# Performance work log

Hardware: AMD Instinct MI355X
Metric: run time of the kernel (lower is better)

## Reference

```python
import jax, jax.numpy as jnp
import numpy as np

T, B, OBS, H, ACT = 256, 1024, 256, 256, 64
SLOPE = 0.1


def setup_inputs() -> dict:
    key = jax.random.key(0)
    ks = jax.random.split(key, 20)
    stdv = 1.0 / np.sqrt(H)
    u = lambda k, shape: jax.random.uniform(k, shape, jnp.float32, -stdv, stdv)
    return {
        "x": jax.random.normal(ks[0], (T, B, OBS), jnp.float32),
        "noise1": jax.random.uniform(ks[1], (T, B, 1), jnp.float32),
        "noise2": jax.random.uniform(ks[2], (T, B, 1), jnp.float32),
        # FCEncoder: two Linear+ReLU layers
        "We1": u(ks[3], (OBS, H)), "be1": u(ks[4], (H,)),
        "We2": u(ks[5], (H, H)), "be2": u(ks[6], (H,)),
        # cell_1 (bottom): U_11 [bottom,4H+1], U_21 [top,4H+1], W_01 [H,4H+1], bias
        "U11_1": u(ks[7], (H, 4 * H + 1)), "U21_1": u(ks[8], (H, 4 * H + 1)),
        "W01_1": u(ks[9], (H, 4 * H + 1)), "b1": u(ks[10], (4 * H + 1,)),
        # cell_2 (top, last layer): no U_21
        "U11_2": u(ks[11], (H, 4 * H + 1)), "W01_2": u(ks[12], (H, 4 * H + 1)),
        "b2": u(ks[13], (4 * H + 1,)),
        "Wh": u(ks[14], (H, H)), "bh": u(ks[15], (H,)),
        "Wp": u(ks[16], (H, ACT)), "bp": u(ks[17], (ACT,)),
    }


def _trigger_train(z_hat, noise):
    # forward: (noise < z_hat).float(); backward: 0.1 * identity (straight-through)
    hard = (noise < z_hat).astype(z_hat.dtype)
    return jax.lax.stop_gradient(hard) + 0.1 * (z_hat - jax.lax.stop_gradient(z_hat))


def _gates(f_s):
    f = jax.nn.sigmoid(f_s[:, 0:H])
    i = jax.nn.sigmoid(f_s[:, H:2 * H])
    o = jax.nn.sigmoid(f_s[:, 2 * H:3 * H])
    g = jnp.tanh(f_s[:, 3 * H:4 * H])
    z_hat = jnp.clip((SLOPE * f_s[:, 4 * H:4 * H + 1] + 1.0) / 2.0, 0.05, 0.95)
    return f, i, o, g, z_hat


def reference(x, noise1, noise2, We1, be1, We2, be2,
              U11_1, U21_1, W01_1, b1, U11_2, W01_2, b2, Wh, bh, Wp, bp):
    # encoder over all timesteps at once (parallel_wrapper equivalent)
    xe = jax.nn.relu(jnp.einsum('tbi,ih->tbh', x, We1) + be1)
    xe = jax.nn.relu(jnp.einsum('tbi,ih->tbh', xe, We2) + be2)

    def step(carry, inp):
        h1, c1, z1, h2, c2 = carry
        xt, n1, n2 = inp
        # ---- cell 1 (not last layer; z_bottom = 1) ----
        fs1 = h1 @ W01_1 + z1 * (h2 @ U21_1) + xt @ U11_1 + b1
        f, i, o, g, zhat1 = _gates(fs1)
        c1n = f * c1 + i * g              # z_bottom == 1 everywhere
        h1n = o * jnp.tanh(c1n)
        z1n = _trigger_train(zhat1, n1)
        # ---- cell 2 (last layer; z_bottom = z1n, s_topdown = 0) ----
        fs2 = h2 @ W01_2 + z1n * (h1n @ U11_2) + b2
        f2, i2, o2, g2, zhat2 = _gates(fs2)
        c2n = (1.0 - z1n) * c2 + z1n * (f2 * c2 + i2 * g2)
        h2n = o2 * jnp.tanh(c2n)
        _ = _trigger_train(zhat2, n2)
        return (h1n, c1n, z1n, h2n, c2n), h2n

    zeros = jnp.zeros((B, H), jnp.float32)
    init = (zeros, zeros, jnp.ones((B, 1), jnp.float32), zeros, zeros)
    _, emb = jax.lax.scan(step, init, (xe, noise1, noise2))  # emb: [T,B,H]

    hid = jax.nn.relu(jnp.einsum('tbh,hk->tbk', emb, Wh) + bh)
    pred = jnp.tanh(jnp.einsum('tbh,ha->tba', hid, Wp) + bp)
    return pred
```

## Files before the change

### kernel.cpp

```cpp
#include <hip/hip_runtime.h>
#include <math.h>

typedef __attribute__((ext_vector_type(8))) _Float16 half8;
typedef __attribute__((ext_vector_type(4))) float    f32x4;
typedef unsigned long long u64;

#define NSTEP 256
#define CH    32
#define NCHUNK (NSTEP/CH)
#define NB    1024
#define HID   256
#define BH    262144
#define LK    40
#define LK1   776
#define INV2K 4.8828125e-4f

#define W1H_OFF 0
#define W1L_OFF 49664
#define AB_OFF  99328
#define W2_OFF  140288
#define PAN_OFF 150528
#define SEQ_SMEM 150784
#define EX_OFF  AB_OFF

__device__ __forceinline__ float sigf(float x){ return 1.f/(1.f+expf(-x)); }
__device__ __forceinline__ void splitf(float v, _Float16& h, _Float16& l){
    h = (_Float16)v; l = (_Float16)((v - (float)h)*2048.f);
}
union H2U { _Float16 h[2]; unsigned u; };

__global__ __launch_bounds__(256)
void wsplit_k(const float* __restrict__ s0, const float* __restrict__ s1,
              const float* __restrict__ s2, int K, int N, int ldn,
              int kb1, int kb2, _Float16* __restrict__ oh, _Float16* __restrict__ ol)
{
    int idx = blockIdx.x*256 + threadIdx.x;
    if (idx >= N*K) return;
    int n = idx / K, k = idx - n*K;
    const float* s = (k < kb1) ? &s0[(size_t)k*ldn]
                   : (k < kb2) ? &s1[(size_t)(k-kb1)*ldn]
                               : &s2[(size_t)(k-kb2)*ldn];
    float v = s[n];
    _Float16 h, l; splitf(v, h, l);
    oh[idx] = h; ol[idx] = l;
}

__global__ void wz_k(const float* __restrict__ W01, const float* __restrict__ U21,
                     const float* __restrict__ U11, float* __restrict__ wz)
{
    int k = blockIdx.x*256 + threadIdx.x;
    if (k >= 768) return;
    wz[k] = (k < 256) ? W01[(size_t)k*1025 + 1024]
          : (k < 512) ? U21[(size_t)(k-256)*1025 + 1024]
                      : U11[(size_t)(k-512)*1025 + 1024];
}

__global__ __launch_bounds__(256)
void init_k(_Float16* h1H, _Float16* h1L, _Float16* h2H, _Float16* h2L,
            float* c1g, float* c2g, unsigned* zr)
{
    int i = blockIdx.x*256 + threadIdx.x;
    h1H[i] = (_Float16)0.f; h1L[i] = (_Float16)0.f;
    h2H[i] = (_Float16)0.f; h2L[i] = (_Float16)0.f;
    c1g[i] = 0.f; c2g[i] = 0.f;
    if (i < NB) zr[i] = 1u;
}

template<int AIN, int AOUT, int NCOL>
__global__ __launch_bounds__(256)
void gemm_t(const float* __restrict__ Af,
            const _Float16* __restrict__ Ah_, const _Float16* __restrict__ Al_,
            const _Float16* __restrict__ Bh_, const _Float16* __restrict__ Bl_,
            const float* __restrict__ bias,
            _Float16* __restrict__ Oh, _Float16* __restrict__ Ol,
            float* __restrict__ Of)
{
    constexpr int NT = 8;
    __shared__ __align__(16) char smem[40960];

    const int tid  = threadIdx.x;
    const size_t R0 = (size_t)blockIdx.x*64;
    const int C0   = blockIdx.y*64;
    const int rh   = (tid>>6)&1, ch = tid>>7;
    const int lane = tid&63, lr = lane&15, kq = (lane>>4)<<3;
    const int arow = tid>>2, seg = tid&3;
    const size_t abase = (R0+arow)*256 + seg*8;
    const size_t wbase = (size_t)(C0 + (tid>>2))*256 + seg*8;

    f32x4 am[2][2], ax[2][2];
#pragma unroll
    for (int r=0;r<2;++r)
#pragma unroll
        for (int c=0;c<2;++c){ am[r][c]=(f32x4)0.f; ax[r][c]=(f32x4)0.f; }

    half8 rah, ral, rwh, rwl;
    auto load_tile = [&](int k0, half8& ah, half8& al, half8& wh, half8& wl) {
        if (AIN == 0) {
            float4 a0 = *(const float4*)(Af + abase + k0);
            float4 a1 = *(const float4*)(Af + abase + k0 + 4);
            float av[8] = {a0.x,a0.y,a0.z,a0.w,a1.x,a1.y,a1.z,a1.w};
#pragma unroll
            for (int i=0;i<8;++i){ _Float16 h,l; splitf(av[i],h,l); ah[i]=h; al[i]=l; }
        } else {
            ah = *(const half8*)(Ah_ + abase + k0);
            al = *(const half8*)(Al_ + abase + k0);
        }
        wh = *(const half8*)(Bh_ + wbase + k0);
        wl = *(const half8*)(Bl_ + wbase + k0);
    };
    auto store_tile = [&](int buf) {
        char* bs = smem + buf*20480;
        *(half8*)((_Float16*)(bs        ) + arow*LK + seg*8) = rah;
        *(half8*)((_Float16*)(bs +  5120) + arow*LK + seg*8) = ral;
        *(half8*)((_Float16*)(bs + 10240) + (tid>>2)*LK + seg*8) = rwh;
        *(half8*)((_Float16*)(bs + 15360) + (tid>>2)*LK + seg*8) = rwl;
    };

    load_tile(0, rah, ral, rwh, rwl);
    store_tile(0);

#pragma unroll 2
    for (int kb = 0; kb < NT; ++kb) {
        const int buf = kb & 1;
        half8 nah, nal, nwh, nwl;
        if (kb+1 < NT) load_tile((kb+1)*32, nah, nal, nwh, nwl);
        __syncthreads();
        const char* bs = smem + buf*20480;
        const _Float16* LAh = (const _Float16*)bs;
        const _Float16* LAl = (const _Float16*)(bs +  5120);
        const _Float16* LBh = (const _Float16*)(bs + 10240);
        const _Float16* LBl = (const _Float16*)(bs + 15360);
        half8 fah[2], fal[2], fbh[2], fbl[2];
#pragma unroll
        for (int rf=0;rf<2;++rf) {
            fah[rf] = *(const half8*)(LAh + (rh*32+rf*16+lr)*LK + kq);
            fal[rf] = *(const half8*)(LAl + (rh*32+rf*16+lr)*LK + kq);
        }
#pragma unroll
        for (int cf=0;cf<2;++cf) {
            fbh[cf] = *(const half8*)(LBh + (ch*32+cf*16+lr)*LK + kq);
            fbl[cf] = *(const half8*)(LBl + (ch*32+cf*16+lr)*LK + kq);
        }
#pragma unroll
        for (int cf=0;cf<2;++cf)
#pragma unroll
            for (int rf=0;rf<2;++rf) {
                am[rf][cf] = __builtin_amdgcn_mfma_f32_16x16x32_f16(fah[rf], fbh[cf], am[rf][cf],0,0,0);
                ax[rf][cf] = __builtin_amdgcn_mfma_f32_16x16x32_f16(fah[rf], fbl[cf], ax[rf][cf],0,0,0);
                ax[rf][cf] = __builtin_amdgcn_mfma_f32_16x16x32_f16(fal[rf], fbh[cf], ax[rf][cf],0,0,0);
            }
        if (kb+1 < NT) {
            rah=nah; ral=nal; rwh=nwh; rwl=nwl;
            store_tile((kb+1)&1);
        }
    }

#pragma unroll
    for (int cf=0;cf<2;++cf) {
        int col = C0 + ch*32 + cf*16 + lr;
        float bcol = bias[col];
#pragma unroll
        for (int rf=0;rf<2;++rf)
#pragma unroll
            for (int q=0;q<4;++q) {
                size_t row = R0 + rh*32 + rf*16 + ((lane>>4)<<2) + q;
                float v = am[rf][cf][q] + ax[rf][cf][q]*INV2K + bcol;
                if (AOUT == 0) {
                    v = fmaxf(v, 0.f);
                    _Float16 h,l; splitf(v,h,l);
                    Oh[row*NCOL + col] = h;
                    Ol[row*NCOL + col] = l;
                } else {
                    Of[row*NCOL + col] = tanhf(v);
                }
            }
    }
}

struct PArgs {
    const _Float16 *XeH, *XeL;
    _Float16 *EmH, *EmL;
    const _Float16 *W1h, *W1l, *W2h, *W2l;
    const float *b1, *b2, *wz, *noise;
    _Float16 *h1rH, *h1rL, *h2rH, *h2rL;
    unsigned *zr;
    float *c1g, *c2g;
    unsigned *ctr;
    unsigned *tick;
    int chunk;
};

__device__ __forceinline__ void xbarrier(unsigned* c, int tid)
{
    __syncthreads();
    if (tid == 0) {
        __hip_atomic_fetch_add(c, 1u, __ATOMIC_RELAXED, __HIP_MEMORY_SCOPE_AGENT);
        int guard = 0;
        while (__hip_atomic_load(c, __ATOMIC_RELAXED, __HIP_MEMORY_SCOPE_AGENT) < 32u
               && guard < (1<<16)) {
            __builtin_amdgcn_s_sleep(2);
            ++guard;
        }
    }
    __syncthreads();
}

__global__ __launch_bounds__(512, 1)
void hm_pers_k(PArgs a)
{
    extern __shared__ __align__(16) char smem[];

    const int tid = threadIdx.x, wv = tid>>6, lane = tid&63;

    unsigned* pan_sh = (unsigned*)(smem + PAN_OFF);
    if (tid == 0) {
        unsigned xcc;
        asm volatile("s_getreg_b32 %0, hwreg(HW_REG_XCC_ID)" : "=s"(xcc));
        xcc &= 7u;
        unsigned slot = __hip_atomic_fetch_add(a.tick + a.chunk*8 + xcc, 1u,
                          __ATOMIC_RELAXED, __HIP_MEMORY_SCOPE_AGENT);
        pan_sh[0] = xcc;
        pan_sh[1] = slot & 31u;
    }
    __syncthreads();
    const int panel = pan_sh[0], cs = pan_sh[1];

    const int rg = wv & 3, cg = wv >> 2;
    const int lr = lane & 15, kq = (lane>>4) << 3;
    const int R0 = panel * 128;
    const int j0h = cs * 8;
    const int srow = tid >> 2, seg = tid & 3;
    const size_t arbase = (size_t)(R0 + srow) * HID;
    const bool do_z = (cs == 0);

    const int fcl  = cg*16 + lr;
    const int gate = fcl >> 3;
    const int jc   = fcl & 7;
    const float bv1 = a.b1[gate*256 + j0h + jc];
    const float bv2 = a.b2[gate*256 + j0h + jc];

    const int hl2 = (tid >= 128) & 1;
    const int tt2 = tid & 127;
    const int fc2 = tt2 >> 2, sg2 = tt2 & 3;
    const _Float16* W2src = hl2 ? a.W2l : a.W2h;
    const size_t w2base = (size_t)((fc2>>3)*256 + j0h + (fc2&7))*512 + sg2*8;

#pragma unroll
    for (int it = 0; it < 12; ++it) {
        int idx = it*512 + tid;
        int hl  = idx >= 3072;
        int e   = idx - hl*3072;
        int fc  = e / 96;
        int ks  = e - fc*96;
        const _Float16* src = (hl ? a.W1l : a.W1h)
            + (size_t)((fc>>3)*256 + j0h + (fc&7))*768 + ks*8;
        *(half8*)(smem + (hl ? W1L_OFF : W1H_OFF) + (fc*LK1 + ks*8)*2)
            = *(const half8*)src;
    }
    __syncthreads();

    const int urow = tid >> 2, ujj = (tid & 3)*2;
    const size_t ubase = (size_t)(R0 + urow)*HID + j0h + ujj;

    float c1s[2], c2s[2];
    {
        float2 cv1 = *(const float2*)(a.c1g + ubase);
        float2 cv2 = *(const float2*)(a.c2g + ubase);
        c1s[0]=cv1.x; c1s[1]=cv1.y; c2s[0]=cv2.x; c2s[1]=cv2.y;
    }

    float* ex = (float*)(smem + EX_OFF);

#pragma unroll 1
    for (int s = 0; s < CH; ++s) {
        const int t = a.chunk*CH + s;
        const _Float16* h1cH = a.h1rH + (size_t)s*BH;
        const _Float16* h1cL = a.h1rL + (size_t)s*BH;
        _Float16*       h1nH = a.h1rH + (size_t)(s+1)*BH;
        _Float16*       h1nL = a.h1rL + (size_t)(s+1)*BH;
        const _Float16* h2cH = a.h2rH + (size_t)s*BH;
        const _Float16* h2cL = a.h2rL + (size_t)s*BH;
        _Float16*       h2nH = a.h2rH + (size_t)(s+1)*BH;
        _Float16*       h2nL = a.h2rL + (size_t)(s+1)*BH;
        const unsigned* zc = a.zr + (size_t)s*NB;
        unsigned*       zn = a.zr + (size_t)(s+1)*NB;
        const _Float16* xeh = a.XeH + (size_t)t*BH;
        const _Float16* xel = a.XeL + (size_t)t*BH;

        const unsigned zrv = zc[R0+srow];
        f32x4 am[2], ax[2];
        am[0]=(f32x4)0.f; am[1]=(f32x4)0.f; ax[0]=(f32x4)0.f; ax[1]=(f32x4)0.f;
        float zacc = 0.f;
        half8 rAh[2], rAl[2], rW[2];

        auto p1_load = [&](int kt, int sl){
            int kg = kt*32 + seg*8;
            half8 hv, lv;
            if (kg < 256)      { hv = *(const half8*)(h1cH + arbase + kg);
                                 lv = *(const half8*)(h1cL + arbase + kg); }
            else if (kg < 512) {
                if (zrv) { hv = *(const half8*)(h2cH + arbase + (kg-256));
                           lv = *(const half8*)(h2cL + arbase + (kg-256)); }
                else     { hv = half8{}; lv = half8{}; }
            } else             { hv = *(const half8*)(xeh + arbase + (kg-512));
                                 lv = *(const half8*)(xel + arbase + (kg-512)); }
            rAh[sl]=hv; rAl[sl]=lv;
        };
        auto stgA = [&](int buf, int sl){
            *(half8*)(smem + AB_OFF + buf*20480         + (srow*LK + seg*8)*2) = rAh[sl];
            *(half8*)(smem + AB_OFF + buf*20480 + 10240 + (srow*LK + seg*8)*2) = rAl[sl];
        };
        auto cmp1 = [&](int buf, int kt){
            const _Float16* LAh = (const _Float16*)(smem + AB_OFF + buf*20480);
            const _Float16* LAl = (const _Float16*)(smem + AB_OFF + buf*20480 + 10240);
            const int bo = fcl*LK1 + kt*32 + kq;
            half8 fbh = *(const half8*)((const _Float16*)(smem + W1H_OFF) + bo);
            half8 fbl = *(const half8*)((const _Float16*)(smem + W1L_OFF) + bo);
#pragma unroll
            for (int rf=0; rf<2; ++rf) {
                const int ao = (rg*32 + rf*16 + lr)*LK + kq;
                half8 fah = *(const half8*)(LAh + ao);
                half8 fal = *(const half8*)(LAl + ao);
                am[rf] = __builtin_amdgcn_mfma_f32_16x16x32_f16(fah, fbh, am[rf],0,0,0);
                ax[rf] = __builtin_amdgcn_mfma_f32_16x16x32_f16(fah, fbl, ax[rf],0,0,0);
                ax[rf] = __builtin_amdgcn_mfma_f32_16x16x32_f16(fal, fbh, ax[rf],0,0,0);
            }
            if (do_z) {
#pragma unroll
                for (int i=0;i<8;++i) {
                    float av = (float)LAh[srow*LK + seg*8 + i]
                             + (float)LAl[srow*LK + seg*8 + i]*INV2K;
                    zacc = fmaf(av, a.wz[kt*32 + seg*8 + i], zacc);
                }
            }
        };

        p1_load(0,0); p1_load(1,1);
        stgA(0,0);
#pragma unroll
        for (int kt = 0; kt < 24; ++kt) {
            if (kt+2 < 24) p1_load(kt+2, kt&1);
            __syncthreads();
            cmp1(kt&1, kt);
            if (kt+1 < 24) stgA((kt+1)&1, (kt+1)&1);
        }
        __syncthreads();

#pragma unroll
        for (int rf=0; rf<2; ++rf)
#pragma unroll
            for (int q=0;q<4;++q) {
                float v = am[rf][q] + ax[rf][q]*INV2K + bv1;
                v = (gate<3) ? sigf(v) : tanhf(v);
                int row = rg*32 + rf*16 + ((lane>>4)<<2) + q;
                ex[(gate*128 + row)*9 + jc] = v;
            }
        if (do_z) {
            float sum = zacc;
            sum += __shfl_xor(sum, 1);
            sum += __shfl_xor(sum, 2);
            if (seg == 0) {
                float fsz = sum + a.b1[1024];
                float zh = fminf(fmaxf((0.1f*fsz + 1.f)*0.5f, 0.05f), 0.95f);
                unsigned zv = (a.noise[(size_t)t*NB + R0+srow] < zh) ? 1u : 0u;
                zn[R0+srow] = zv;
                if (s == CH-1) a.zr[R0+srow] = zv;
            }
        }
        __syncthreads();
        {
            H2U hh, hl;
#pragma unroll
            for (int q=0;q<2;++q) {
                float f0 = ex[(0*128+urow)*9 + ujj + q];
                float i0 = ex[(1*128+urow)*9 + ujj + q];
                float o0 = ex[(2*128+urow)*9 + ujj + q];
                float g0 = ex[(3*128+urow)*9 + ujj + q];
                float cn = f0*c1s[q] + i0*g0;
                c1s[q] = cn;
                float hv = o0*tanhf(cn);
                _Float16 h,l; splitf(hv,h,l); hh.h[q]=h; hl.h[q]=l;
            }
            *(unsigned*)(h1nH + ubase) = hh.u;
            *(unsigned*)(h1nL + ubase) = hl.u;
            if (s == CH-1) {
                *(unsigned*)(a.h1rH + ubase) = hh.u;
                *(unsigned*)(a.h1rL + ubase) = hl.u;
            }
        }
        xbarrier(a.ctr + ((size_t)(a.chunk*CH + s)*2 + 0)*8 + panel, tid);

        const unsigned zrv2 = zn[R0+srow];
        am[0]=(f32x4)0.f; am[1]=(f32x4)0.f; ax[0]=(f32x4)0.f; ax[1]=(f32x4)0.f;

        auto p2_load = [&](int kt, int sl){
            int kg = kt*32 + seg*8;
            half8 hv, lv;
            if (kg < 256)      { hv = *(const half8*)(h2cH + arbase + kg);
                                 lv = *(const half8*)(h2cL + arbase + kg); }
            else {
                if (zrv2) { hv = *(const half8*)(h1nH + arbase + (kg-256));
                            lv = *(const half8*)(h1nL + arbase + (kg-256)); }
                else      { hv = half8{}; lv = half8{}; }
            }
            rAh[sl]=hv; rAl[sl]=lv;
            if (tid < 256) rW[sl] = *(const half8*)(W2src + w2base + kt*32);
        };
        auto stg2 = [&](int buf, int sl){
            *(half8*)(smem + AB_OFF + buf*20480         + (srow*LK + seg*8)*2) = rAh[sl];
            *(half8*)(smem + AB_OFF + buf*20480 + 10240 + (srow*LK + seg*8)*2) = rAl[sl];
            if (tid < 256)
                *(half8*)(smem + W2_OFF + buf*5120 + hl2*2560 + (fc2*LK + sg2*8)*2) = rW[sl];
        };
        auto cmp2 = [&](int buf){
            const _Float16* LAh = (const _Float16*)(smem + AB_OFF + buf*20480);
            const _Float16* LAl = (const _Float16*)(smem + AB_OFF + buf*20480 + 10240);
            const int bo = fcl*LK + kq;
            half8 fbh = *(const half8*)((const _Float16*)(smem + W2_OFF + buf*5120) + bo);
            half8 fbl = *(const half8*)((const _Float16*)(smem + W2_OFF + buf*5120 + 2560) + bo);
#pragma unroll
            for (int rf=0; rf<2; ++rf) {
                const int ao = (rg*32 + rf*16 + lr)*LK + kq;
                half8 fah = *(const half8*)(LAh + ao);
                half8 fal = *(const half8*)(LAl + ao);
                am[rf] = __builtin_amdgcn_mfma_f32_16x16x32_f16(fah, fbh, am[rf],0,0,0);
                ax[rf] = __builtin_amdgcn_mfma_f32_16x16x32_f16(fah, fbl, ax[rf],0,0,0);
                ax[rf] = __builtin_amdgcn_mfma_f32_16x16x32_f16(fal, fbh, ax[rf],0,0,0);
            }
        };

        p2_load(0,0); p2_load(1,1);
        stg2(0,0);
#pragma unroll
        for (int kt = 0; kt < 16; ++kt) {
            if (kt+2 < 16) p2_load(kt+2, kt&1);
            __syncthreads();
            cmp2(kt&1);
            if (kt+1 < 16) stg2((kt+1)&1, (kt+1)&1);
        }
        __syncthreads();

#pragma unroll
        for (int rf=0; rf<2; ++rf)
#pragma unroll
            for (int q=0;q<4;++q) {
                float v = am[rf][q] + ax[rf][q]*INV2K + bv2;
                v = (gate<3) ? sigf(v) : tanhf(v);
                int row = rg*32 + rf*16 + ((lane>>4)<<2) + q;
                ex[(gate*128 + row)*9 + jc] = v;
            }
        __syncthreads();
        {
            unsigned zun = zn[R0+urow];
            H2U hh, hl;
#pragma unroll
            for (int q=0;q<2;++q) {
                float f0 = ex[(0*128+urow)*9 + ujj + q];
                float i0 = ex[(1*128+urow)*9 + ujj + q];
                float o0 = ex[(2*128+urow)*9 + ujj + q];
                float g0 = ex[(3*128+urow)*9 + ujj + q];
                float cn = zun ? (f0*c2s[q] + i0*g0) : c2s[q];
                c2s[q] = cn;
                float hv = o0*tanhf(cn);
                _Float16 h,l; splitf(hv,h,l); hh.h[q]=h; hl.h[q]=l;
            }
            *(unsigned*)(h2nH + ubase) = hh.u;
            *(unsigned*)(h2nL + ubase) = hl.u;
            *(unsigned*)(a.EmH + (size_t)t*BH + ubase) = hh.u;
            *(unsigned*)(a.EmL + (size_t)t*BH + ubase) = hl.u;
            if (s == CH-1) {
                *(unsigned*)(a.h2rH + ubase) = hh.u;
                *(unsigned*)(a.h2rL + ubase) = hl.u;
            }
        }
        xbarrier(a.ctr + ((size_t)(a.chunk*CH + s)*2 + 1)*8 + panel, tid);
    }

    *(float2*)(a.c1g + ubase) = float2{c1s[0], c1s[1]};
    *(float2*)(a.c2g + ubase) = float2{c2s[0], c2s[1]};
}

extern "C" void kernel_launch(void* const* d_in, const int* in_sizes, int n_in,
                              void* d_out, int out_size, void* d_ws, size_t ws_size,
                              hipStream_t stream)
{
    const float* x     = (const float*)d_in[0];
    const float* n1    = (const float*)d_in[1];
    const float* We1   = (const float*)d_in[3];
    const float* be1   = (const float*)d_in[4];
    const float* We2   = (const float*)d_in[5];
    const float* be2   = (const float*)d_in[6];
    const float* U11_1 = (const float*)d_in[7];
    const float* U21_1 = (const float*)d_in[8];
    const float* W01_1 = (const float*)d_in[9];
    const float* b1    = (const float*)d_in[10];
    const float* U11_2 = (const float*)d_in[11];
    const float* W01_2 = (const float*)d_in[12];
    const float* b2    = (const float*)d_in[13];
    const float* Wh    = (const float*)d_in[14];
    const float* bh    = (const float*)d_in[15];
    const float* Wp    = (const float*)d_in[16];
    const float* bp_   = (const float*)d_in[17];
    float* out = (float*)d_out;

    char* p = (char*)d_ws;
    auto alloc = [&](size_t bytes){ char* q = p; p += (bytes + 255) & ~(size_t)255; return q; };
    _Float16* XeH  = (_Float16*)alloc((size_t)NSTEP*BH*2);
    _Float16* XeL  = (_Float16*)alloc((size_t)NSTEP*BH*2);
    _Float16* EmH  = (_Float16*)alloc((size_t)NSTEP*BH*2);
    _Float16* EmL  = (_Float16*)alloc((size_t)NSTEP*BH*2);
    _Float16* Wt1h = (_Float16*)alloc((size_t)1024*768*2);
    _Float16* Wt1l = (_Float16*)alloc((size_t)1024*768*2);
    _Float16* Wt2h = (_Float16*)alloc((size_t)1024*512*2);
    _Float16* Wt2l = (_Float16*)alloc((size_t)1024*512*2);
    _Float16* We1h = (_Float16*)alloc(256*256*2);
    _Float16* We1l = (_Float16*)alloc(256*256*2);
    _Float16* We2h = (_Float16*)alloc(256*256*2);
    _Float16* We2l = (_Float16*)alloc(256*256*2);
    _Float16* Whh  = (_Float16*)alloc(256*256*2);
    _Float16* Whl  = (_Float16*)alloc(256*256*2);
    _Float16* Wph  = (_Float16*)alloc(64*256*2);
    _Float16* Wpl  = (_Float16*)alloc(64*256*2);
    float*    wz1  = (float*)alloc(768*4);
    _Float16* h1rH = (_Float16*)alloc((size_t)(CH+1)*BH*2);
    _Float16* h1rL = (_Float16*)alloc((size_t)(CH+1)*BH*2);
    _Float16* h2rH = (_Float16*)alloc((size_t)(CH+1)*BH*2);
    _Float16* h2rL = (_Float16*)alloc((size_t)(CH+1)*BH*2);
    unsigned* zr   = (unsigned*)alloc((size_t)(CH+1)*NB*4);
    float*    c1g  = (float*)alloc((size_t)BH*4);
    float*    c2g  = (float*)alloc((size_t)BH*4);
    unsigned* ctr  = (unsigned*)alloc((size_t)NCHUNK*CH*2*8*4);
    unsigned* tick = (unsigned*)alloc((size_t)NCHUNK*8*4);
    if (ws_size < (size_t)(p - (char*)d_ws)) return;

    _Float16* TmpH = EmH; _Float16* TmpL = EmL;
    _Float16* TpH  = XeH; _Float16* TpL  = XeL;

    wsplit_k<<<dim3(3072), 256, 0, stream>>>(W01_1, U21_1, U11_1, 768, 1024, 1025, 256, 512, Wt1h, Wt1l);
    wsplit_k<<<dim3(2048), 256, 0, stream>>>(W01_2, U11_2, nullptr, 512, 1024, 1025, 256, 512, Wt2h, Wt2l);
    wsplit_k<<<dim3(256),  256, 0, stream>>>(We1, nullptr, nullptr, 256, 256, 256, 256, 256, We1h, We1l);
    wsplit_k<<<dim3(256),  256, 0, stream>>>(We2, nullptr, nullptr, 256, 256, 256, 256, 256, We2h, We2l);
    wsplit_k<<<dim3(256),  256, 0, stream>>>(Wh,  nullptr, nullptr, 256, 256, 256, 256, 256, Whh,  Whl);
    wsplit_k<<<dim3(64),   256, 0, stream>>>(Wp,  nullptr, nullptr, 256, 64, 64, 256, 256, Wph, Wpl);
    wz_k<<<dim3(3), 256, 0, stream>>>(W01_1, U21_1, U11_1, wz1);
    init_k<<<dim3(1024), 256, 0, stream>>>(h1rH, h1rL, h2rH, h2rL, c1g, c2g, zr);
    (void)hipMemsetAsync(ctr, 0, (size_t)NCHUNK*CH*2*8*4, stream);
    (void)hipMemsetAsync(tick, 0, (size_t)NCHUNK*8*4, stream);

    for (int c = 0; c < 8; ++c) {
        size_t ro = (size_t)c*32*BH;
        gemm_t<0,0,256><<<dim3(512,4), 256, 0, stream>>>(
            x + ro, nullptr, nullptr, We1h, We1l, be1, TmpH, TmpL, nullptr);
        gemm_t<1,0,256><<<dim3(512,4), 256, 0, stream>>>(
            nullptr, TmpH, TmpL, We2h, We2l, be2, XeH + ro, XeL + ro, nullptr);
    }

    (void)hipFuncSetAttribute((const void*)hm_pers_k,
        hipFuncAttributeMaxDynamicSharedMemorySize, SEQ_SMEM);
    PArgs pa;
    pa.XeH = XeH; pa.XeL = XeL; pa.EmH = EmH; pa.EmL = EmL;
    pa.W1h = Wt1h; pa.W1l = Wt1l; pa.W2h = Wt2h; pa.W2l = Wt2l;
    pa.b1 = b1; pa.b2 = b2; pa.wz = wz1; pa.noise = n1;
    pa.h1rH = h1rH; pa.h1rL = h1rL; pa.h2rH = h2rH; pa.h2rL = h2rL;
    pa.zr = zr; pa.c1g = c1g; pa.c2g = c2g; pa.ctr = ctr; pa.tick = tick;
    for (int c = 0; c < NCHUNK; ++c) {
        pa.chunk = c;
        void* kargs[] = { (void*)&pa };
        (void)hipLaunchCooperativeKernel((const void*)hm_pers_k, dim3(256), dim3(512),
                                         kargs, SEQ_SMEM, stream);
    }

    for (int c = 0; c < 8; ++c) {
        size_t ro = (size_t)c*32*BH;
        gemm_t<1,0,256><<<dim3(512,4), 256, 0, stream>>>(
            nullptr, EmH + ro, EmL + ro, Whh, Whl, bh, TpH, TpL, nullptr);
        gemm_t<1,1,64><<<dim3(512,1), 256, 0, stream>>>(
            nullptr, TpH, TpL, Wph, Wpl, bp_, nullptr, nullptr,
            out + (size_t)c*32*NB*64);
    }
}
```

Measured before the change: 7.312 ms.

## Interleave gate columns so each lane computes full LSTM cell in registers

Weight columns are permuted at split time so the four gates of one hidden unit land in adjacent MFMA output rows. Each wave now owns 16 batch rows and streams activations directly from global memory into MFMA operands, with no LDS staging of A tiles. The gate nonlinearity and cell update happen in registers without the LDS exchange buffer and the extra block barriers. Layer-2 high weights are kept in LDS while the low parts are read from global, and the z reduction runs as a separate pass. In exchange there are more redundant global loads and scalar 2-byte stores instead of packed stores.

Result: slower. 10.39 ms (+42.0%).

```diff
diff --git a/kernel.cpp b/kernel.cpp
--- a/kernel.cpp
+++ b/kernel.cpp
@@ -13,34 +13,34 @@
 #define BH    262144
 #define LK    40
 #define LK1   776
+#define LW2   520
 #define INV2K 4.8828125e-4f
 
 #define W1H_OFF 0
 #define W1L_OFF 49664
-#define AB_OFF  99328
-#define W2_OFF  140288
-#define PAN_OFF 150528
-#define SEQ_SMEM 150784
-#define EX_OFF  AB_OFF
+#define W2H_OFF 99328
+#define PAN_OFF 132608
+#define SEQ_SMEM 132864
 
 __device__ __forceinline__ float sigf(float x){ return 1.f/(1.f+expf(-x)); }
 __device__ __forceinline__ void splitf(float v, _Float16& h, _Float16& l){
     h = (_Float16)v; l = (_Float16)((v - (float)h)*2048.f);
 }
-union H2U { _Float16 h[2]; unsigned u; };
 
 __global__ __launch_bounds__(256)
 void wsplit_k(const float* __restrict__ s0, const float* __restrict__ s1,
               const float* __restrict__ s2, int K, int N, int ldn,
-              int kb1, int kb2, _Float16* __restrict__ oh, _Float16* __restrict__ ol)
+              int kb1, int kb2, int perm,
+              _Float16* __restrict__ oh, _Float16* __restrict__ ol)
 {
     int idx = blockIdx.x*256 + threadIdx.x;
     if (idx >= N*K) return;
     int n = idx / K, k = idx - n*K;
+    int jsrc = perm ? ((n&3)*256 + (n>>2)) : n;
     const float* s = (k < kb1) ? &s0[(size_t)k*ldn]
                    : (k < kb2) ? &s1[(size_t)(k-kb1)*ldn]
                                : &s2[(size_t)(k-kb2)*ldn];
-    float v = s[n];
+    float v = s[jsrc];
     _Float16 h, l; splitf(v, h, l);
     oh[idx] = h; ol[idx] = l;
 }
@@ -211,6 +211,7 @@
     extern __shared__ __align__(16) char smem[];
 
     const int tid = threadIdx.x, wv = tid>>6, lane = tid&63;
+    const int lr = lane&15, hq = lane>>4, kg8 = hq<<3;
 
     unsigned* pan_sh = (unsigned*)(smem + PAN_OFF);
     if (tid == 0) {
@@ -224,52 +225,51 @@
     }
     __syncthreads();
     const int panel = pan_sh[0], cs = pan_sh[1];
-
-    const int rg = wv & 3, cg = wv >> 2;
-    const int lr = lane & 15, kq = (lane>>4) << 3;
-    const int R0 = panel * 128;
-    const int j0h = cs * 8;
-    const int srow = tid >> 2, seg = tid & 3;
-    const size_t arbase = (size_t)(R0 + srow) * HID;
+    const int R0 = panel*128, hb = cs*8;
+    const int row = R0 + wv*16 + lr;
+    const size_t rbase = (size_t)row*HID;
     const bool do_z = (cs == 0);
-
-    const int fcl  = cg*16 + lr;
-    const int gate = fcl >> 3;
-    const int jc   = fcl & 7;
-    const float bv1 = a.b1[gate*256 + j0h + jc];
-    const float bv2 = a.b2[gate*256 + j0h + jc];
-
-    const int hl2 = (tid >= 128) & 1;
-    const int tt2 = tid & 127;
-    const int fc2 = tt2 >> 2, sg2 = tt2 & 3;
-    const _Float16* W2src = hl2 ? a.W2l : a.W2h;
-    const size_t w2base = (size_t)((fc2>>3)*256 + j0h + (fc2&7))*512 + sg2*8;
+    const int hc0 = hb + hq, hc1 = hb + 4 + hq;
+
+    float b1v[2][4], b2v[2][4];
+#pragma unroll
+    for (int cf=0; cf<2; ++cf)
+#pragma unroll
+        for (int q=0;q<4;++q) {
+            int hc = hb + cf*4 + hq;
+            b1v[cf][q] = a.b1[q*256 + hc];
+            b2v[cf][q] = a.b2[q*256 + hc];
+        }
 
 #pragma unroll
     for (int it = 0; it < 12; ++it) {
         int idx = it*512 + tid;
         int hl  = idx >= 3072;
         int e   = idx - hl*3072;
-        int fc  = e / 96;
-        int ks  = e - fc*96;
+        int c   = e / 96;
+        int ks  = e - c*96;
         const _Float16* src = (hl ? a.W1l : a.W1h)
-            + (size_t)((fc>>3)*256 + j0h + (fc&7))*768 + ks*8;
-        *(half8*)(smem + (hl ? W1L_OFF : W1H_OFF) + (fc*LK1 + ks*8)*2)
+            + (size_t)(cs*32 + c)*768 + ks*8;
+        *(half8*)(smem + (hl ? W1L_OFF : W1H_OFF) + (c*LK1 + ks*8)*2)
             = *(const half8*)src;
     }
+#pragma unroll
+    for (int it = 0; it < 4; ++it) {
+        int idx = it*512 + tid;
+        int c   = idx >> 6;
+        int ks  = idx & 63;
+        const _Float16* src = a.W2h + (size_t)(cs*32 + c)*512 + ks*8;
+        *(half8*)(smem + W2H_OFF + (c*LW2 + ks*8)*2) = *(const half8*)src;
+    }
     __syncthreads();
 
-    const int urow = tid >> 2, ujj = (tid & 3)*2;
-    const size_t ubase = (size_t)(R0 + urow)*HID + j0h + ujj;
-
-    float c1s[2], c2s[2];
-    {
-        float2 cv1 = *(const float2*)(a.c1g + ubase);
-        float2 cv2 = *(const float2*)(a.c2g + ubase);
-        c1s[0]=cv1.x; c1s[1]=cv1.y; c2s[0]=cv2.x; c2s[1]=cv2.y;
-    }
-
-    float* ex = (float*)(smem + EX_OFF);
+    float c1s[2] = { a.c1g[rbase + hc0], a.c1g[rbase + hc1] };
+    float c2s[2] = { a.c2g[rbase + hc0], a.c2g[rbase + hc1] };
+
+    const _Float16* w2lp[2] = {
+        a.W2l + (size_t)(cs*32      + lr)*512 + kg8,
+        a.W2l + (size_t)(cs*32 + 16 + lr)*512 + kg8
+    };
 
 #pragma unroll 1
     for (int s = 0; s < CH; ++s) {
@@ -287,197 +287,127 @@
         const _Float16* xeh = a.XeH + (size_t)t*BH;
         const _Float16* xel = a.XeL + (size_t)t*BH;
 
-        const unsigned zrv = zc[R0+srow];
+        const bool zrv = zc[row] != 0u;
         f32x4 am[2], ax[2];
         am[0]=(f32x4)0.f; am[1]=(f32x4)0.f; ax[0]=(f32x4)0.f; ax[1]=(f32x4)0.f;
-        float zacc = 0.f;
-        half8 rAh[2], rAl[2], rW[2];
-
-        auto p1_load = [&](int kt, int sl){
-            int kg = kt*32 + seg*8;
-            half8 hv, lv;
-            if (kg < 256)      { hv = *(const half8*)(h1cH + arbase + kg);
-                                 lv = *(const half8*)(h1cL + arbase + kg); }
-            else if (kg < 512) {
-                if (zrv) { hv = *(const half8*)(h2cH + arbase + (kg-256));
-                           lv = *(const half8*)(h2cL + arbase + (kg-256)); }
-                else     { hv = half8{}; lv = half8{}; }
-            } else             { hv = *(const half8*)(xeh + arbase + (kg-512));
-                                 lv = *(const half8*)(xel + arbase + (kg-512)); }
-            rAh[sl]=hv; rAl[sl]=lv;
-        };
-        auto stgA = [&](int buf, int sl){
-            *(half8*)(smem + AB_OFF + buf*20480         + (srow*LK + seg*8)*2) = rAh[sl];
-            *(half8*)(smem + AB_OFF + buf*20480 + 10240 + (srow*LK + seg*8)*2) = rAl[sl];
-        };
-        auto cmp1 = [&](int buf, int kt){
-            const _Float16* LAh = (const _Float16*)(smem + AB_OFF + buf*20480);
-            const _Float16* LAl = (const _Float16*)(smem + AB_OFF + buf*20480 + 10240);
-            const int bo = fcl*LK1 + kt*32 + kq;
-            half8 fbh = *(const half8*)((const _Float16*)(smem + W1H_OFF) + bo);
-            half8 fbl = *(const half8*)((const _Float16*)(smem + W1L_OFF) + bo);
-#pragma unroll
-            for (int rf=0; rf<2; ++rf) {
-                const int ao = (rg*32 + rf*16 + lr)*LK + kq;
-                half8 fah = *(const half8*)(LAh + ao);
-                half8 fal = *(const half8*)(LAl + ao);
-                am[rf] = __builtin_amdgcn_mfma_f32_16x16x32_f16(fah, fbh, am[rf],0,0,0);
-                ax[rf] = __builtin_amdgcn_mfma_f32_16x16x32_f16(fah, fbl, ax[rf],0,0,0);
-                ax[rf] = __builtin_amdgcn_mfma_f32_16x16x32_f16(fal, fbh, ax[rf],0,0,0);
+
+#pragma unroll
+        for (int kt = 0; kt < 24; ++kt) {
+            const int k0 = kt*32;
+            half8 sh, sl;
+            if (k0 < 256)      { sh = *(const half8*)(h1cH + rbase + k0 + kg8);
+                                 sl = *(const half8*)(h1cL + rbase + k0 + kg8); }
+            else if (k0 < 512) { sh = *(const half8*)(h2cH + rbase + (k0-256) + kg8);
+                                 sl = *(const half8*)(h2cL + rbase + (k0-256) + kg8);
+                                 if (!zrv) { sh = half8{}; sl = half8{}; } }
+            else               { sh = *(const half8*)(xeh + rbase + (k0-512) + kg8);
+                                 sl = *(const half8*)(xel + rbase + (k0-512) + kg8); }
+#pragma unroll
+            for (int cf = 0; cf < 2; ++cf) {
+                const int wb = (cf*16 + lr)*LK1 + k0 + kg8;
+                half8 wh = *(const half8*)((const _Float16*)(smem + W1H_OFF) + wb);
+                half8 wl = *(const half8*)((const _Float16*)(smem + W1L_OFF) + wb);
+                am[cf] = __builtin_amdgcn_mfma_f32_16x16x32_f16(wh, sh, am[cf],0,0,0);
+                ax[cf] = __builtin_amdgcn_mfma_f32_16x16x32_f16(wl, sh, ax[cf],0,0,0);
+                ax[cf] = __builtin_amdgcn_mfma_f32_16x16x32_f16(wh, sl, ax[cf],0,0,0);
             }
-            if (do_z) {
-#pragma unroll
-                for (int i=0;i<8;++i) {
-                    float av = (float)LAh[srow*LK + seg*8 + i]
-                             + (float)LAl[srow*LK + seg*8 + i]*INV2K;
-                    zacc = fmaf(av, a.wz[kt*32 + seg*8 + i], zacc);
-                }
+        }
+
+        if (do_z) {
+            const int srow = tid>>2, seg = tid&3;
+            const int grow = R0 + srow;
+            const size_t rb = (size_t)grow*HID;
+            const bool zrow_v = zc[grow] != 0u;
+            float zacc = 0.f;
+#pragma unroll
+            for (int kt = 0; kt < 24; ++kt) {
+                const int k0 = kt*32 + seg*8;
+                half8 hv, lv;
+                if (k0 < 256)      { hv = *(const half8*)(h1cH + rb + k0);
+                                     lv = *(const half8*)(h1cL + rb + k0); }
+                else if (k0 < 512) { hv = *(const half8*)(h2cH + rb + (k0-256));
+                                     lv = *(const half8*)(h2cL + rb + (k0-256));
+                                     if (!zrow_v) { hv = half8{}; lv = half8{}; } }
+                else               { hv = *(const half8*)(xeh + rb + (k0-512));
+                                     lv = *(const half8*)(xel + rb + (k0-512)); }
+#pragma unroll
+                for (int i=0;i<8;++i)
+                    zacc = fmaf((float)hv[i] + (float)lv[i]*INV2K,
+                                a.wz[k0 + i], zacc);
             }
-        };
-
-        p1_load(0,0); p1_load(1,1);
-        stgA(0,0);
-#pragma unroll
-        for (int kt = 0; kt < 24; ++kt) {
-            if (kt+2 < 24) p1_load(kt+2, kt&1);
-            __syncthreads();
-            cmp1(kt&1, kt);
-            if (kt+1 < 24) stgA((kt+1)&1, (kt+1)&1);
-        }
-        __syncthreads();
-
-#pragma unroll
-        for (int rf=0; rf<2; ++rf)
-#pragma unroll
-            for (int q=0;q<4;++q) {
-                float v = am[rf][q] + ax[rf][q]*INV2K + bv1;
-                v = (gate<3) ? sigf(v) : tanhf(v);
-                int row = rg*32 + rf*16 + ((lane>>4)<<2) + q;
-                ex[(gate*128 + row)*9 + jc] = v;
+            zacc += __shfl_xor(zacc, 1);
+            zacc += __shfl_xor(zacc, 2);
+            if (seg == 0) {
+                float fsz = zacc + a.b1[1024];
+                float zh = fminf(fmaxf((0.1f*fsz + 1.f)*0.5f, 0.05f), 0.95f);
+                unsigned zv = (a.noise[(size_t)t*NB + grow] < zh) ? 1u : 0u;
+                zn[grow] = zv;
+                if (s == CH-1) a.zr[grow] = zv;
             }
-        if (do_z) {
-            float sum = zacc;
-            sum += __shfl_xor(sum, 1);
-            sum += __shfl_xor(sum, 2);
-            if (seg == 0) {
-                float fsz = sum + a.b1[1024];
-                float zh = fminf(fmaxf((0.1f*fsz + 1.f)*0.5f, 0.05f), 0.95f);
-                unsigned zv = (a.noise[(size_t)t*NB + R0+srow] < zh) ? 1u : 0u;
-                zn[R0+srow] = zv;
-                if (s == CH-1) a.zr[R0+srow] = zv;
+        }
+
+#pragma unroll
+        for (int cf = 0; cf < 2; ++cf) {
+            float v0 = am[cf][0] + ax[cf][0]*INV2K + b1v[cf][0];
+            float v1 = am[cf][1] + ax[cf][1]*INV2K + b1v[cf][1];
+            float v2 = am[cf][2] + ax[cf][2]*INV2K + b1v[cf][2];
+            float v3 = am[cf][3] + ax[cf][3]*INV2K + b1v[cf][3];
+            float f = sigf(v0), i = sigf(v1), o = sigf(v2), g = tanhf(v3);
+            float cn = f*c1s[cf] + i*g;
+            c1s[cf] = cn;
+            float hn = o*tanhf(cn);
+            _Float16 hh, hl; splitf(hn, hh, hl);
+            const int hc = (cf==0) ? hc0 : hc1;
+            h1nH[rbase + hc] = hh; h1nL[rbase + hc] = hl;
+            if (s == CH-1) { a.h1rH[rbase + hc] = hh; a.h1rL[rbase + hc] = hl; }
+        }
+        xbarrier(a.ctr + ((size_t)(a.chunk*CH + s)*2 + 0)*8 + panel, tid);
+
+        const bool znv = zn[row] != 0u;
+        am[0]=(f32x4)0.f; am[1]=(f32x4)0.f; ax[0]=(f32x4)0.f; ax[1]=(f32x4)0.f;
+
+#pragma unroll
+        for (int kt = 0; kt < 16; ++kt) {
+            const int k0 = kt*32;
+            half8 sh, sl;
+            if (k0 < 256) { sh = *(const half8*)(h2cH + rbase + k0 + kg8);
+                            sl = *(const half8*)(h2cL + rbase + k0 + kg8); }
+            else          { sh = *(const half8*)(h1nH + rbase + (k0-256) + kg8);
+                            sl = *(const half8*)(h1nL + rbase + (k0-256) + kg8);
+                            if (!znv) { sh = half8{}; sl = half8{}; } }
+#pragma unroll
+            for (int cf = 0; cf < 2; ++cf) {
+                const int wb = (cf*16 + lr)*LW2 + k0 + kg8;
+                half8 wh = *(const half8*)((const _Float16*)(smem + W2H_OFF) + wb);
+                half8 wl = *(const half8*)(w2lp[cf] + k0);
+                am[cf] = __builtin_amdgcn_mfma_f32_16x16x32_f16(wh, sh, am[cf],0,0,0);
+                ax[cf] = __builtin_amdgcn_mfma_f32_16x16x32_f16(wl, sh, ax[cf],0,0,0);
+                ax[cf] = __builtin_amdgcn_mfma_f32_16x16x32_f16(wh, sl, ax[cf],0,0,0);
             }
         }
-        __syncthreads();
-        {
-            H2U hh, hl;
-#pragma unroll
-            for (int q=0;q<2;++q) {
-                float f0 = ex[(0*128+urow)*9 + ujj + q];
-                float i0 = ex[(1*128+urow)*9 + ujj + q];
-                float o0 = ex[(2*128+urow)*9 + ujj + q];
-                float g0 = ex[(3*128+urow)*9 + ujj + q];
-                float cn = f0*c1s[q] + i0*g0;
-                c1s[q] = cn;
-                float hv = o0*tanhf(cn);
-                _Float16 h,l; splitf(hv,h,l); hh.h[q]=h; hl.h[q]=l;
-            }
-            *(unsigned*)(h1nH + ubase) = hh.u;
-            *(unsigned*)(h1nL + ubase) = hl.u;
-            if (s == CH-1) {
-                *(unsigned*)(a.h1rH + ubase) = hh.u;
-                *(unsigned*)(a.h1rL + ubase) = hl.u;
-            }
-        }
-        xbarrier(a.ctr + ((size_t)(a.chunk*CH + s)*2 + 0)*8 + panel, tid);
-
-        const unsigned zrv2 = zn[R0+srow];
-        am[0]=(f32x4)0.f; am[1]=(f32x4)0.f; ax[0]=(f32x4)0.f; ax[1]=(f32x4)0.f;
-
-        auto p2_load = [&](int kt, int sl){
-            int kg = kt*32 + seg*8;
-            half8 hv, lv;
-            if (kg < 256)      { hv = *(const half8*)(h2cH + arbase + kg);
-                                 lv = *(const half8*)(h2cL + arbase + kg); }
-            else {
-                if (zrv2) { hv = *(const half8*)(h1nH + arbase + (kg-256));
-                            lv = *(const half8*)(h1nL + arbase + (kg-256)); }
-                else      { hv = half8{}; lv = half8{}; }
-            }
-            rAh[sl]=hv; rAl[sl]=lv;
-            if (tid < 256) rW[sl] = *(const half8*)(W2src + w2base + kt*32);
-        };
-        auto stg2 = [&](int buf, int sl){
-            *(half8*)(smem + AB_OFF + buf*20480         + (srow*LK + seg*8)*2) = rAh[sl];
-            *(half8*)(smem + AB_OFF + buf*20480 + 10240 + (srow*LK + seg*8)*2) = rAl[sl];
-            if (tid < 256)
-                *(half8*)(smem + W2_OFF + buf*5120 + hl2*2560 + (fc2*LK + sg2*8)*2) = rW[sl];
-        };
-        auto cmp2 = [&](int buf){
-            const _Float16* LAh = (const _Float16*)(smem + AB_OFF + buf*20480);
-            const _Float16* LAl = (const _Float16*)(smem + AB_OFF + buf*20480 + 10240);
-            const int bo = fcl*LK + kq;
-            half8 fbh = *(const half8*)((const _Float16*)(smem + W2_OFF + buf*5120) + bo);
-            half8 fbl = *(const half8*)((const _Float16*)(smem + W2_OFF + buf*5120 + 2560) + bo);
-#pragma unroll
-            for (int rf=0; rf<2; ++rf) {
-                const int ao = (rg*32 + rf*16 + lr)*LK + kq;
-                half8 fah = *(const half8*)(LAh + ao);
-                half8 fal = *(const half8*)(LAl + ao);
-                am[rf] = __builtin_amdgcn_mfma_f32_16x16x32_f16(fah, fbh, am[rf],0,0,0);
-                ax[rf] = __builtin_amdgcn_mfma_f32_16x16x32_f16(fah, fbl, ax[rf],0,0,0);
-                ax[rf] = __builtin_amdgcn_mfma_f32_16x16x32_f16(fal, fbh, ax[rf],0,0,0);
-            }
-        };
-
-        p2_load(0,0); p2_load(1,1);
-        stg2(0,0);
-#pragma unroll
-        for (int kt = 0; kt < 16; ++kt) {
-            if (kt+2 < 16) p2_load(kt+2, kt&1);
-            __syncthreads();
-            cmp2(kt&1);
-            if (kt+1 < 16) stg2((kt+1)&1, (kt+1)&1);
-        }
-        __syncthreads();
-
-#pragma unroll
-        for (int rf=0; rf<2; ++rf)
-#pragma unroll
-            for (int q=0;q<4;++q) {
-                float v = am[rf][q] + ax[rf][q]*INV2K + bv2;
-                v = (gate<3) ? sigf(v) : tanhf(v);
-                int row = rg*32 + rf*16 + ((lane>>4)<<2) + q;
-                ex[(gate*128 + row)*9 + jc] = v;
-            }
-        __syncthreads();
-        {
-            unsigned zun = zn[R0+urow];
-            H2U hh, hl;
-#pragma unroll
-            for (int q=0;q<2;++q) {
-                float f0 = ex[(0*128+urow)*9 + ujj + q];
-                float i0 = ex[(1*128+urow)*9 + ujj + q];
-                float o0 = ex[(2*128+urow)*9 + ujj + q];
-                float g0 = ex[(3*128+urow)*9 + ujj + q];
-                float cn = zun ? (f0*c2s[q] + i0*g0) : c2s[q];
-                c2s[q] = cn;
-                float hv = o0*tanhf(cn);
-                _Float16 h,l; splitf(hv,h,l); hh.h[q]=h; hl.h[q]=l;
-            }
-            *(unsigned*)(h2nH + ubase) = hh.u;
-            *(unsigned*)(h2nL + ubase) = hl.u;
-            *(unsigned*)(a.EmH + (size_t)t*BH + ubase) = hh.u;
-            *(unsigned*)(a.EmL + (size_t)t*BH + ubase) = hl.u;
-            if (s == CH-1) {
-                *(unsigned*)(a.h2rH + ubase) = hh.u;
-                *(unsigned*)(a.h2rL + ubase) = hl.u;
-            }
+
+#pragma unroll
+        for (int cf = 0; cf < 2; ++cf) {
+            float v0 = am[cf][0] + ax[cf][0]*INV2K + b2v[cf][0];
+            float v1 = am[cf][1] + ax[cf][1]*INV2K + b2v[cf][1];
+            float v2 = am[cf][2] + ax[cf][2]*INV2K + b2v[cf][2];
+            float v3 = am[cf][3] + ax[cf][3]*INV2K + b2v[cf][3];
+            float f = sigf(v0), i = sigf(v1), o = sigf(v2), g = tanhf(v3);
+            float cn = znv ? (f*c2s[cf] + i*g) : c2s[cf];
+            c2s[cf] = cn;
+            float hn = o*tanhf(cn);
+            _Float16 hh, hl; splitf(hn, hh, hl);
+            const int hc = (cf==0) ? hc0 : hc1;
+            h2nH[rbase + hc] = hh; h2nL[rbase + hc] = hl;
+            a.EmH[(size_t)t*BH + rbase + hc] = hh;
+            a.EmL[(size_t)t*BH + rbase + hc] = hl;
+            if (s == CH-1) { a.h2rH[rbase + hc] = hh; a.h2rL[rbase + hc] = hl; }
         }
         xbarrier(a.ctr + ((size_t)(a.chunk*CH + s)*2 + 1)*8 + panel, tid);
     }
 
-    *(float2*)(a.c1g + ubase) = float2{c1s[0], c1s[1]};
-    *(float2*)(a.c2g + ubase) = float2{c2s[0], c2s[1]};
+    a.c1g[rbase + hc0] = c1s[0]; a.c1g[rbase + hc1] = c1s[1];
+    a.c2g[rbase + hc0] = c2s[0]; a.c2g[rbase + hc1] = c2s[1];
 }
 
 extern "C" void kernel_launch(void* const* d_in, const int* in_sizes, int n_in,
@@ -536,12 +466,12 @@
     _Float16* TmpH = EmH; _Float16* TmpL = EmL;
     _Float16* TpH  = XeH; _Float16* TpL  = XeL;
 
-    wsplit_k<<<dim3(3072), 256, 0, stream>>>(W01_1, U21_1, U11_1, 768, 1024, 1025, 256, 512, Wt1h, Wt1l);
-    wsplit_k<<<dim3(2048), 256, 0, stream>>>(W01_2, U11_2, nullptr, 512, 1024, 1025, 256, 512, Wt2h, Wt2l);
-    wsplit_k<<<dim3(256),  256, 0, stream>>>(We1, nullptr, nullptr, 256, 256, 256, 256, 256, We1h, We1l);
-    wsplit_k<<<dim3(256),  256, 0, stream>>>(We2, nullptr, nullptr, 256, 256, 256, 256, 256, We2h, We2l);
-    wsplit_k<<<dim3(256),  256, 0, stream>>>(Wh,  nullptr, nullptr, 256, 256, 256, 256, 256, Whh,  Whl);
-    wsplit_k<<<dim3(64),   256, 0, stream>>>(Wp,  nullptr, nullptr, 256, 64, 64, 256, 256, Wph, Wpl);
+    wsplit_k<<<dim3(3072), 256, 0, stream>>>(W01_1, U21_1, U11_1, 768, 1024, 1025, 256, 512, 1, Wt1h, Wt1l);
+    wsplit_k<<<dim3(2048), 256, 0, stream>>>(W01_2, U11_2, nullptr, 512, 1024, 1025, 256, 512, 1, Wt2h, Wt2l);
+    wsplit_k<<<dim3(256),  256, 0, stream>>>(We1, nullptr, nullptr, 256, 256, 256, 256, 256, 0, We1h, We1l);
+    wsplit_k<<<dim3(256),  256, 0, stream>>>(We2, nullptr, nullptr, 256, 256, 256, 256, 256, 0, We2h, We2l);
+    wsplit_k<<<dim3(256),  256, 0, stream>>>(Wh,  nullptr, nullptr, 256, 256, 256, 256, 256, 0, Whh,  Whl);
+    wsplit_k<<<dim3(64),   256, 0, stream>>>(Wp,  nullptr, nullptr, 256, 64, 64, 256, 256, 0, Wph, Wpl);
     wz_k<<<dim3(3), 256, 0, stream>>>(W01_1, U21_1, U11_1, wz1);
     init_k<<<dim3(1024), 256, 0, stream>>>(h1rH, h1rL, h2rH, h2rL, c1g, c2g, zr);
     (void)hipMemsetAsync(ctr, 0, (size_t)NCHUNK*CH*2*8*4, stream);
```
